# Kernel tuning notes

Measured on AMD Instinct MI355X. Metric: run time of the kernel, lower is better.

Reference implementation:

```python
import jax, jax.numpy as jnp
import numpy as np

EPS = 1e-5
ALPHA = 0.2  # leaky relu negative slope


def instance_norm(x):
    # x: [b, n, c]; torch InstanceNorm1d normalizes each (b, c) over the n dim (no affine)
    mean = jnp.mean(x, axis=1, keepdims=True)
    var = jnp.var(x, axis=1, keepdims=True)
    return (x - mean) * jax.lax.rsqrt(var + EPS)


def gat_layer(x, w, a_src, a_dst, bias):
    # x: [b, n, f_in], w: [h, f_in, f_out], a_src/a_dst: [h, f_out, 1], bias: [f_out]
    h_prime = jnp.einsum('bnf,hfo->bhno', x, w)              # [b, h, n, f_out]
    attn_src = jnp.einsum('bhno,hoi->bhni', h_prime, a_src)[..., 0]  # [b, h, n]
    attn_dst = jnp.einsum('bhno,hoi->bhni', h_prime, a_dst)[..., 0]  # [b, h, n]
    # outer-sum additive attention: attn[b,h,i,j] = src[b,h,i] + dst[b,h,j]
    attn = attn_src[:, :, :, None] + attn_dst[:, :, None, :]
    attn = jnp.where(attn >= 0, attn, ALPHA * attn)          # leaky relu
    attn = jax.nn.softmax(attn, axis=-1)
    out = jnp.einsum('bhnm,bhmo->bhno', attn, h_prime) + bias
    return out


def setup_inputs() -> dict:
    key = jax.random.key(0)
    ks = jax.random.split(key, 9)
    b, n = 16, 1024
    f0, f1, f2 = 32, 16, 32   # n_units
    h0, h1 = 4, 1             # n_heads

    def xavier(k, shape, gain=1.414):
        fan_in, fan_out = shape[-2], shape[-1]
        a = gain * np.sqrt(6.0 / (fan_in + fan_out))
        return jax.random.uniform(k, shape, jnp.float32, -a, a)

    return {
        'x': jax.random.normal(ks[0], (b, n, f0), jnp.float32),
        'w1': xavier(ks[1], (h0, f0, f1)),
        'a_src1': xavier(ks[2], (h0, f1, 1)),
        'a_dst1': xavier(ks[3], (h0, f1, 1)),
        'b1': jnp.zeros((f1,), jnp.float32),
        'w2': xavier(ks[4], (h1, f1 * h0, f2)),
        'a_src2': xavier(ks[5], (h1, f2, 1)),
        'a_dst2': xavier(ks[6], (h1, f2, 1)),
        'b2': jnp.zeros((f2,), jnp.float32),
    }


def reference(x, w1, a_src1, a_dst1, b1, w2, a_src2, a_dst2, b2):
    b, n = x.shape[:2]
    # layer 0
    x = instance_norm(x)
    out = gat_layer(x, w1, a_src1, a_dst1, b1)               # [b, h0, n, f1]
    x = jnp.transpose(out, (0, 2, 1, 3)).reshape(b, n, -1)   # [b, n, h0*f1]
    x = jax.nn.elu(x)
    # layer 1 (last): squeeze head dim
    x = instance_norm(x)
    out = gat_layer(x, w2, a_src2, a_dst2, b2)               # [b, 1, n, f2]
    return out[:, 0]                                          # [b, n, f2]
```

## Files before the change

### kernel.cpp

```cpp
#include <hip/hip_runtime.h>


namespace {
constexpr int Nn  = 1024;
constexpr int F0  = 32;
constexpr int F1n = 16;
constexpr int FH  = 64;
constexpr int F2n = 32;
constexpr float LOG2E = 1.4426950408889634f;
constexpr float EPS   = 1e-5f;
constexpr float ALPHA = 0.2f;
}

typedef __attribute__((ext_vector_type(8))) _Float16 half8;
typedef __attribute__((ext_vector_type(4))) float f32x4;

union alignas(16) Smem {
  struct { float sum[8][33], ssq[8][33], mean[32], rstd[32], wt[2048], as[64], ad[64]; } p1;
  struct { float dst[Nn], red[4], ps[4][16]; } p2;
  struct { float mean[64], rstd[64], wt[2048], as[32], ad[32], sd[4][64][2]; } p3;
  struct { float dst[Nn], red[4], comb[3][64][9], ps[16]; } p4;
};

__device__ __forceinline__ void grid_barrier(unsigned* c, unsigned nblk) {
  __syncthreads();
  if (threadIdx.x == 0) {
    __threadfence();
    __hip_atomic_fetch_add(c, 1u, __ATOMIC_RELAXED, __HIP_MEMORY_SCOPE_AGENT);
    while (__hip_atomic_load(c, __ATOMIC_RELAXED, __HIP_MEMORY_SCOPE_AGENT) < nblk)
      __builtin_amdgcn_s_sleep(2);
    __threadfence();
  }
  __syncthreads();
}

__device__ __forceinline__ void proj1_body(
    int bid, int t, Smem& sm,
    const float* __restrict__ x, const float* __restrict__ w1,
    const float* __restrict__ asrc, const float* __restrict__ adst,
    short* __restrict__ hpT_hi, short* __restrict__ hpT_lo,
    float* __restrict__ src, float* __restrict__ dst,
    float* __restrict__ statsAcc)
{
  const int b    = bid >> 4;
  const int tile = bid & 15;
  const int r    = t & 63, h = t >> 6;

  if (tile == 0 && t < 128) statsAcc[b * 128 + t] = 0.f;

  for (int idx = t; idx < 4 * F1n * F0; idx += 256) {
    const int f = idx & 31, ho = idx >> 5;
    sm.p1.wt[idx] = w1[((ho >> 4) * F0 + f) * F1n + (ho & 15)];
  }
  if (t < 64) { sm.p1.as[t] = asrc[t]; sm.p1.ad[t] = adst[t]; }

  const float* xb = x + (size_t)b * Nn * F0;
  {
    const int c = t & 31, seg = t >> 5;
    float sum = 0.f, ssq = 0.f;
#pragma unroll 8
    for (int nn = seg; nn < Nn; nn += 8) {
      float v = xb[nn * F0 + c];
      sum += v; ssq += v * v;
    }
    sm.p1.sum[seg][c] = sum; sm.p1.ssq[seg][c] = ssq;
  }
  __syncthreads();
  if (t < 32) {
    float s = 0.f, q = 0.f;
#pragma unroll
    for (int k = 0; k < 8; k++) { s += sm.p1.sum[k][t]; q += sm.p1.ssq[k][t]; }
    const float mean = s * (1.f / Nn);
    const float var  = fmaf(-mean, mean, q * (1.f / Nn));
    sm.p1.mean[t] = mean;
    sm.p1.rstd[t] = rsqrtf(var + EPS);
  }
  __syncthreads();

  const int n  = tile * 64 + r;
  const int bh = b * 4 + h;
  float4 xr[F0 / 4];
  const float4* xrow = reinterpret_cast<const float4*>(xb + (size_t)n * F0);
#pragma unroll
  for (int k = 0; k < F0 / 4; k++) {
    float4 v = xrow[k];
    v.x = (v.x - sm.p1.mean[k * 4 + 0]) * sm.p1.rstd[k * 4 + 0];
    v.y = (v.y - sm.p1.mean[k * 4 + 1]) * sm.p1.rstd[k * 4 + 1];
    v.z = (v.z - sm.p1.mean[k * 4 + 2]) * sm.p1.rstd[k * 4 + 2];
    v.w = (v.w - sm.p1.mean[k * 4 + 3]) * sm.p1.rstd[k * 4 + 3];
    xr[k] = v;
  }

  const float4* wt4 = reinterpret_cast<const float4*>(sm.p1.wt);
  float sdot = 0.f, ddot = 0.f;
#pragma unroll 1
  for (int o = 0; o < F1n; o++) {
    float acc = 0.f;
#pragma unroll
    for (int k = 0; k < F0 / 4; k++) {
      const float4 wv = wt4[(h * F1n + o) * (F0 / 4) + k];
      const float4 xv = xr[k];
      acc = fmaf(xv.x, wv.x, acc); acc = fmaf(xv.y, wv.y, acc);
      acc = fmaf(xv.z, wv.z, acc); acc = fmaf(xv.w, wv.w, acc);
    }
    sdot = fmaf(acc, sm.p1.as[h * F1n + o], sdot);
    ddot = fmaf(acc, sm.p1.ad[h * F1n + o], ddot);
    const _Float16 hh = (_Float16)acc;
    const _Float16 hl = (_Float16)(acc - (float)hh);
    const size_t idx = ((size_t)bh * F1n + o) * Nn + n;
    hpT_hi[idx] = __builtin_bit_cast(short, hh);
    hpT_lo[idx] = __builtin_bit_cast(short, hl);
  }
  src[bh * Nn + n] = sdot;
  dst[bh * Nn + n] = ddot;
}

__device__ __forceinline__ void attn1_body(
    int bid, int t, Smem& sm,
    const short* __restrict__ hpT_hi, const short* __restrict__ hpT_lo,
    const float* __restrict__ src, const float* __restrict__ dst,
    const float* __restrict__ bias, float* __restrict__ x1,
    float* __restrict__ statsAcc)
{
  const int bh   = bid >> 4;
  const int tile = bid & 15;
  const int w    = t >> 6;
  const int l    = t & 63;
  const int col  = l & 15;
  const int ks   = l >> 4;

  const float* dp = dst + bh * Nn;
  float lm = -1e30f;
  for (int j = t; j < Nn; j += 256) { float v = dp[j]; sm.p2.dst[j] = v; lm = fmaxf(lm, v); }
#pragma unroll
  for (int mask = 32; mask >= 1; mask >>= 1) lm = fmaxf(lm, __shfl_xor(lm, mask));
  if (l == 0) sm.p2.red[w] = lm;
  __syncthreads();
  const float dmax = fmaxf(fmaxf(sm.p2.red[0], sm.p2.red[1]),
                           fmaxf(sm.p2.red[2], sm.p2.red[3]));

  const int i0 = tile * 64 + w * 16;
  const float si = src[bh * Nn + i0 + col];
  const float t0v = si + dmax;
  const float em  = fmaxf(t0v, ALPHA * t0v) * LOG2E;

  auto pexp = [&](float dv) {
    const float tt = si + dv;
    const float u  = fmaxf(tt, ALPHA * tt);
    return exp2f(fmaf(u, LOG2E, -em));
  };

  const half8* bph = reinterpret_cast<const half8*>(hpT_hi + (size_t)bh * F1n * Nn);
  const half8* bpl = reinterpret_cast<const half8*>(hpT_lo + (size_t)bh * F1n * Nn);
  f32x4 acc = {0.f, 0.f, 0.f, 0.f};
  float psum = 0.f;

#pragma unroll 2
  for (int jb = 0; jb < 32; ++jb) {
    const int jo = (jb << 5) | (ks << 3);
    const float4 dA = *reinterpret_cast<const float4*>(&sm.p2.dst[jo]);
    const float4 dB = *reinterpret_cast<const float4*>(&sm.p2.dst[jo + 4]);
    half8 af;
    const _Float16 q0 = (_Float16)pexp(dA.x); af[0] = q0;
    const _Float16 q1 = (_Float16)pexp(dA.y); af[1] = q1;
    const _Float16 q2 = (_Float16)pexp(dA.z); af[2] = q2;
    const _Float16 q3 = (_Float16)pexp(dA.w); af[3] = q3;
    const _Float16 q4 = (_Float16)pexp(dB.x); af[4] = q4;
    const _Float16 q5 = (_Float16)pexp(dB.y); af[5] = q5;
    const _Float16 q6 = (_Float16)pexp(dB.z); af[6] = q6;
    const _Float16 q7 = (_Float16)pexp(dB.w); af[7] = q7;
    psum += (((float)q0 + (float)q1) + ((float)q2 + (float)q3)) +
            (((float)q4 + (float)q5) + ((float)q6 + (float)q7));

    const half8 bh8 = bph[col * 128 + (jb << 2) + ks];
    const half8 bl8 = bpl[col * 128 + (jb << 2) + ks];
    acc = __builtin_amdgcn_mfma_f32_16x16x32_f16(af, bh8, acc, 0, 0, 0);
    acc = __builtin_amdgcn_mfma_f32_16x16x32_f16(af, bl8, acc, 0, 0, 0);
  }

  psum += __shfl_xor(psum, 16);
  psum += __shfl_xor(psum, 32);
  if (l < 16) sm.p2.ps[w][col] = psum;
  __syncthreads();

  const int b = bh >> 2, h = bh & 3;
  const float bc = bias[col];
  float sv = 0.f, sq = 0.f;
#pragma unroll
  for (int r = 0; r < 4; ++r) {
    const int row = ks * 4 + r;
    const float inv = 1.f / sm.p2.ps[w][row];
    float v = fmaf(acc[r], inv, bc);
    v = v > 0.f ? v : exp2f(v * LOG2E) - 1.f;
    x1[((size_t)(b * Nn + i0 + row)) * FH + h * F1n + col] = v;
    sv += v; sq += v * v;
  }
  sv += __shfl_xor(sv, 16); sq += __shfl_xor(sq, 16);
  sv += __shfl_xor(sv, 32); sq += __shfl_xor(sq, 32);
  if (l < 16) {
    const int ch = h * F1n + col;
    atomicAdd(&statsAcc[b * 128 + ch], sv);
    atomicAdd(&statsAcc[b * 128 + 64 + ch], sq);
  }
}

__device__ __forceinline__ void proj2_body(
    int bid, int t, Smem& sm,
    const float* __restrict__ x1, const float* __restrict__ statsAcc,
    const float* __restrict__ w2,
    const float* __restrict__ asrc, const float* __restrict__ adst,
    short* __restrict__ hpT_hi, short* __restrict__ hpT_lo,
    float* __restrict__ src, float* __restrict__ dst)
{
  const int b    = bid >> 4;
  const int tile = bid & 15;
  const int r    = t & 63, og = t >> 6;

  for (int idx = t; idx < F2n * FH; idx += 256) {
    const int f = idx & 63, o = idx >> 6;
    sm.p3.wt[idx] = w2[f * F2n + o];
  }
  if (t < F2n) { sm.p3.as[t] = asrc[t]; sm.p3.ad[t] = adst[t]; }
  if (t < 64) {
    const float s = statsAcc[b * 128 + t];
    const float q = statsAcc[b * 128 + 64 + t];
    const float mean = s * (1.f / Nn);
    const float var  = fmaf(-mean, mean, q * (1.f / Nn));
    sm.p3.mean[t] = mean;
    sm.p3.rstd[t] = rsqrtf(var + EPS);
  }
  __syncthreads();

  const int n    = tile * 64 + r;
  const int base = b * Nn + n;
  float4 xr[FH / 4];
  const float4* xrow = reinterpret_cast<const float4*>(
      x1 + (size_t)b * Nn * FH + (size_t)n * FH);
#pragma unroll
  for (int k = 0; k < FH / 4; k++) {
    float4 v = xrow[k];
    v.x = (v.x - sm.p3.mean[k * 4 + 0]) * sm.p3.rstd[k * 4 + 0];
    v.y = (v.y - sm.p3.mean[k * 4 + 1]) * sm.p3.rstd[k * 4 + 1];
    v.z = (v.z - sm.p3.mean[k * 4 + 2]) * sm.p3.rstd[k * 4 + 2];
    v.w = (v.w - sm.p3.mean[k * 4 + 3]) * sm.p3.rstd[k * 4 + 3];
    xr[k] = v;
  }

  const float4* wt4 = reinterpret_cast<const float4*>(sm.p3.wt);
  float sdot = 0.f, ddot = 0.f;
#pragma unroll 1
  for (int oo = 0; oo < 8; oo++) {
    const int o = og * 8 + oo;
    float acc = 0.f;
#pragma unroll
    for (int k = 0; k < FH / 4; k++) {
      const float4 wv = wt4[o * (FH / 4) + k];
      const float4 xv = xr[k];
      acc = fmaf(xv.x, wv.x, acc); acc = fmaf(xv.y, wv.y, acc);
      acc = fmaf(xv.z, wv.z, acc); acc = fmaf(xv.w, wv.w, acc);
    }
    sdot = fmaf(acc, sm.p3.as[o], sdot);
    ddot = fmaf(acc, sm.p3.ad[o], ddot);
    const _Float16 hh = (_Float16)acc;
    const _Float16 hl = (_Float16)(acc - (float)hh);
    const size_t idx = ((size_t)b * F2n + o) * Nn + n;
    hpT_hi[idx] = __builtin_bit_cast(short, hh);
    hpT_lo[idx] = __builtin_bit_cast(short, hl);
  }

  sm.p3.sd[og][r][0] = sdot; sm.p3.sd[og][r][1] = ddot;
  __syncthreads();
  if (og == 0) {
    float s = 0.f, d = 0.f;
#pragma unroll
    for (int g = 0; g < 4; g++) { s += sm.p3.sd[g][r][0]; d += sm.p3.sd[g][r][1]; }
    src[base] = s;
    dst[base] = d;
  }
}

__device__ __forceinline__ void attn2_body(
    int bid, int t, Smem& sm,
    const short* __restrict__ hpT_hi, const short* __restrict__ hpT_lo,
    const float* __restrict__ src, const float* __restrict__ dst,
    const float* __restrict__ bias, float* __restrict__ out)
{
  const int b    = bid >> 6;
  const int tile = bid & 63;
  const int jq   = t >> 6;
  const int l    = t & 63;
  const int col  = l & 15;
  const int ks   = l >> 4;

  const float* dp = dst + b * Nn;
  float lm = -1e30f;
  for (int j = t; j < Nn; j += 256) { float v = dp[j]; sm.p4.dst[j] = v; lm = fmaxf(lm, v); }
#pragma unroll
  for (int mask = 32; mask >= 1; mask >>= 1) lm = fmaxf(lm, __shfl_xor(lm, mask));
  if (l == 0) sm.p4.red[jq] = lm;
  __syncthreads();
  const float dmax = fmaxf(fmaxf(sm.p4.red[0], sm.p4.red[1]),
                           fmaxf(sm.p4.red[2], sm.p4.red[3]));

  const int i0 = tile * 16;
  const float si = src[b * Nn + i0 + col];
  const float t0v = si + dmax;
  const float em  = fmaxf(t0v, ALPHA * t0v) * LOG2E;

  auto pexp = [&](float dv) {
    const float tt = si + dv;
    const float u  = fmaxf(tt, ALPHA * tt);
    return exp2f(fmaf(u, LOG2E, -em));
  };

  const half8* bph = reinterpret_cast<const half8*>(hpT_hi + (size_t)b * F2n * Nn);
  const half8* bpl = reinterpret_cast<const half8*>(hpT_lo + (size_t)b * F2n * Nn);
  f32x4 acc0 = {0.f, 0.f, 0.f, 0.f};
  f32x4 acc1 = {0.f, 0.f, 0.f, 0.f};
  float psum = 0.f;

#pragma unroll 2
  for (int kb = 0; kb < 8; ++kb) {
    const int jb = jq * 8 + kb;
    const int jo = (jb << 5) | (ks << 3);
    const float4 dA = *reinterpret_cast<const float4*>(&sm.p4.dst[jo]);
    const float4 dB = *reinterpret_cast<const float4*>(&sm.p4.dst[jo + 4]);
    half8 af;
    const _Float16 q0 = (_Float16)pexp(dA.x); af[0] = q0;
    const _Float16 q1 = (_Float16)pexp(dA.y); af[1] = q1;
    const _Float16 q2 = (_Float16)pexp(dA.z); af[2] = q2;
    const _Float16 q3 = (_Float16)pexp(dA.w); af[3] = q3;
    const _Float16 q4 = (_Float16)pexp(dB.x); af[4] = q4;
    const _Float16 q5 = (_Float16)pexp(dB.y); af[5] = q5;
    const _Float16 q6 = (_Float16)pexp(dB.z); af[6] = q6;
    const _Float16 q7 = (_Float16)pexp(dB.w); af[7] = q7;
    psum += (((float)q0 + (float)q1) + ((float)q2 + (float)q3)) +
            (((float)q4 + (float)q5) + ((float)q6 + (float)q7));

    const half8 bh0 = bph[col * 128 + (jb << 2) + ks];
    const half8 bl0 = bpl[col * 128 + (jb << 2) + ks];
    const half8 bh1 = bph[(col + 16) * 128 + (jb << 2) + ks];
    const half8 bl1 = bpl[(col + 16) * 128 + (jb << 2) + ks];
    acc0 = __builtin_amdgcn_mfma_f32_16x16x32_f16(af, bh0, acc0, 0, 0, 0);
    acc0 = __builtin_amdgcn_mfma_f32_16x16x32_f16(af, bl0, acc0, 0, 0, 0);
    acc1 = __builtin_amdgcn_mfma_f32_16x16x32_f16(af, bh1, acc1, 0, 0, 0);
    acc1 = __builtin_amdgcn_mfma_f32_16x16x32_f16(af, bl1, acc1, 0, 0, 0);
  }

  if (jq > 0) {
#pragma unroll
    for (int r = 0; r < 4; ++r) {
      sm.p4.comb[jq - 1][l][r]     = acc0[r];
      sm.p4.comb[jq - 1][l][r + 4] = acc1[r];
    }
    sm.p4.comb[jq - 1][l][8] = psum;
  }
  __syncthreads();

  if (jq == 0) {
#pragma unroll
    for (int g = 0; g < 3; ++g) {
#pragma unroll
      for (int r = 0; r < 4; ++r) {
        acc0[r] += sm.p4.comb[g][l][r];
        acc1[r] += sm.p4.comb[g][l][r + 4];
      }
      psum += sm.p4.comb[g][l][8];
    }
    psum += __shfl_xor(psum, 16);
    psum += __shfl_xor(psum, 32);
    if (l < 16) sm.p4.ps[col] = psum;

    const float bc0 = bias[col];
    const float bc1 = bias[col + 16];
#pragma unroll
    for (int r = 0; r < 4; ++r) {
      const int row = ks * 4 + r;
      const float inv = 1.f / sm.p4.ps[row];
      float* op = out + ((size_t)(b * Nn + i0 + row)) * F2n;
      op[col]      = fmaf(acc0[r], inv, bc0);
      op[col + 16] = fmaf(acc1[r], inv, bc1);
    }
  }
}

__global__ __launch_bounds__(256, 4) void k_fused(
    const float* __restrict__ x, const float* __restrict__ w1,
    const float* __restrict__ as1, const float* __restrict__ ad1,
    const float* __restrict__ b1,  const float* __restrict__ w2,
    const float* __restrict__ as2, const float* __restrict__ ad2,
    const float* __restrict__ b2,
    short* hpT1_hi, short* hpT1_lo, short* hpT2_hi, short* hpT2_lo,
    float* x1, float* src1, float* dst1, float* src2, float* dst2,
    float* statsA, float* out, unsigned* bars)
{
  __shared__ Smem sm;
  const int bid = blockIdx.x, t = threadIdx.x;

  if (bid < 256)
    proj1_body(bid, t, sm, x, w1, as1, ad1, hpT1_hi, hpT1_lo, src1, dst1, statsA);
  grid_barrier(bars + 0, 1024u);

  attn1_body(bid, t, sm, hpT1_hi, hpT1_lo, src1, dst1, b1, x1, statsA);
  grid_barrier(bars + 1, 1024u);

  if (bid < 256)
    proj2_body(bid, t, sm, x1, statsA, w2, as2, ad2, hpT2_hi, hpT2_lo, src2, dst2);
  grid_barrier(bars + 2, 1024u);

  attn2_body(bid, t, sm, hpT2_hi, hpT2_lo, src2, dst2, b2, out);
}

__global__ __launch_bounds__(256) void k_proj1(
    const float* x, const float* w1, const float* as1, const float* ad1,
    short* hpT_hi, short* hpT_lo, float* src, float* dst, float* statsA)
{ __shared__ Smem sm; proj1_body(blockIdx.x, threadIdx.x, sm, x, w1, as1, ad1, hpT_hi, hpT_lo, src, dst, statsA); }

__global__ __launch_bounds__(256) void k_attn1(
    const short* hpT_hi, const short* hpT_lo, const float* src, const float* dst,
    const float* bias, float* x1, float* statsA)
{ __shared__ Smem sm; attn1_body(blockIdx.x, threadIdx.x, sm, hpT_hi, hpT_lo, src, dst, bias, x1, statsA); }

__global__ __launch_bounds__(256) void k_proj2(
    const float* x1, const float* statsA, const float* w2,
    const float* as2, const float* ad2,
    short* hpT_hi, short* hpT_lo, float* src, float* dst)
{ __shared__ Smem sm; proj2_body(blockIdx.x, threadIdx.x, sm, x1, statsA, w2, as2, ad2, hpT_hi, hpT_lo, src, dst); }

__global__ __launch_bounds__(256) void k_attn2(
    const short* hpT_hi, const short* hpT_lo, const float* src, const float* dst,
    const float* bias, float* out)
{ __shared__ Smem sm; attn2_body(blockIdx.x, threadIdx.x, sm, hpT_hi, hpT_lo, src, dst, bias, out); }

extern "C" void kernel_launch(void* const* d_in, const int* in_sizes, int n_in,
                              void* d_out, int out_size, void* d_ws, size_t ws_size,
                              hipStream_t stream) {
  (void)in_sizes; (void)n_in; (void)out_size; (void)ws_size;
  const float* x   = (const float*)d_in[0];
  const float* w1  = (const float*)d_in[1];
  const float* as1 = (const float*)d_in[2];
  const float* ad1 = (const float*)d_in[3];
  const float* b1  = (const float*)d_in[4];
  const float* w2  = (const float*)d_in[5];
  const float* as2 = (const float*)d_in[6];
  const float* ad2 = (const float*)d_in[7];
  const float* b2  = (const float*)d_in[8];
  float* out = (float*)d_out;

  float* ws = (float*)d_ws;
  short* hpT1_hi = (short*)ws;
  short* hpT1_lo = (short*)(ws + 524288);
  short* hpT2_hi = (short*)(ws + 1048576);
  short* hpT2_lo = (short*)(ws + 1048576 + 262144);
  float* x1      = ws + 1048576 + 524288;
  float* src1    = x1 + 1048576;
  float* dst1    = src1 + 65536;
  float* src2    = dst1 + 65536;
  float* dst2    = src2 + 16384;
  float* statsA  = dst2 + 16384;
  unsigned* bars = (unsigned*)(statsA + 2048);

  (void)hipMemsetAsync(bars, 0, 3 * sizeof(unsigned), stream);

  int maxB = 0;
  hipError_t e = hipOccupancyMaxActiveBlocksPerMultiprocessor(&maxB, k_fused, 256, 0);
  if (e == hipSuccess && maxB >= 4) {
    k_fused<<<1024, 256, 0, stream>>>(x, w1, as1, ad1, b1, w2, as2, ad2, b2,
                                      hpT1_hi, hpT1_lo, hpT2_hi, hpT2_lo,
                                      x1, src1, dst1, src2, dst2, statsA, out, bars);
  } else {
    k_proj1<<<256, 256, 0, stream>>>(x, w1, as1, ad1, hpT1_hi, hpT1_lo, src1, dst1, statsA);
    k_attn1<<<1024, 256, 0, stream>>>(hpT1_hi, hpT1_lo, src1, dst1, b1, x1, statsA);
    k_proj2<<<256, 256, 0, stream>>>(x1, statsA, w2, as2, ad2, hpT2_hi, hpT2_lo, src2, dst2);
    k_attn2<<<1024, 256, 0, stream>>>(hpT2_hi, hpT2_lo, src2, dst2, b2, out);
  }
}
```

Baseline: 146.0 us.

## Replace grid-wide barriers with per-batch barriers and spread projections over all blocks

The fused kernel's three grid-wide barriers over 1024 blocks become per-batch barriers, each counting only the 64 blocks of one batch, with counters padded 32 words apart. Blocks of a batch can then move to the next phase without waiting for the whole grid. Both projection phases now run on all 1024 blocks at 16 rows each, instead of 256 blocks at 64 rows, so no blocks sit idle. Each block stages its normalized rows in shared memory and reduces partial attention dots with wave shuffles. In exchange, every block still recomputes the instance-norm statistics over the full batch, which means four times as many redundant reads of the inputs.

```diff
diff --git a/kernel.cpp b/kernel.cpp
--- a/kernel.cpp
+++ b/kernel.cpp
@@ -16,37 +16,35 @@
 typedef __attribute__((ext_vector_type(4))) float f32x4;
 
 union alignas(16) Smem {
-  struct { float sum[8][33], ssq[8][33], mean[32], rstd[32], wt[2048], as[64], ad[64]; } p1;
+  struct { float sum[8][33], ssq[8][33], mean[32], rstd[32], wt[2048], as[64], ad[64], x[16][33]; } p1;
   struct { float dst[Nn], red[4], ps[4][16]; } p2;
-  struct { float mean[64], rstd[64], wt[2048], as[32], ad[32], sd[4][64][2]; } p3;
+  struct { float mean[64], rstd[64], wt[2048], as[32], ad[32], x[16][65]; } p3;
   struct { float dst[Nn], red[4], comb[3][64][9], ps[16]; } p4;
 };
 
-__device__ __forceinline__ void grid_barrier(unsigned* c, unsigned nblk) {
+__device__ __forceinline__ void batch_barrier(unsigned* c) {
   __syncthreads();
   if (threadIdx.x == 0) {
     __threadfence();
     __hip_atomic_fetch_add(c, 1u, __ATOMIC_RELAXED, __HIP_MEMORY_SCOPE_AGENT);
-    while (__hip_atomic_load(c, __ATOMIC_RELAXED, __HIP_MEMORY_SCOPE_AGENT) < nblk)
-      __builtin_amdgcn_s_sleep(2);
+    while (__hip_atomic_load(c, __ATOMIC_RELAXED, __HIP_MEMORY_SCOPE_AGENT) < 64u)
+      __builtin_amdgcn_s_sleep(1);
     __threadfence();
   }
   __syncthreads();
 }
 
 __device__ __forceinline__ void proj1_body(
-    int bid, int t, Smem& sm,
+    int b, int u, int t, Smem& sm,
     const float* __restrict__ x, const float* __restrict__ w1,
     const float* __restrict__ asrc, const float* __restrict__ adst,
     short* __restrict__ hpT_hi, short* __restrict__ hpT_lo,
     float* __restrict__ src, float* __restrict__ dst,
     float* __restrict__ statsAcc)
 {
-  const int b    = bid >> 4;
-  const int tile = bid & 15;
-  const int r    = t & 63, h = t >> 6;
-
-  if (tile == 0 && t < 128) statsAcc[b * 128 + t] = 0.f;
+  const int r = t >> 4, h = (t >> 2) & 3, dup = t & 3;
+
+  if (u == 0 && t < 128) statsAcc[b * 128 + t] = 0.f;
 
   for (int idx = t; idx < 4 * F1n * F0; idx += 256) {
     const int f = idx & 31, ho = idx >> 5;
@@ -77,61 +75,56 @@
   }
   __syncthreads();
 
-  const int n  = tile * 64 + r;
+  const int n0 = u * 16;
+  for (int idx = t; idx < 16 * F0; idx += 256) {
+    const int rr = idx >> 5, f = idx & 31;
+    sm.p1.x[rr][f] = (xb[(n0 + rr) * F0 + f] - sm.p1.mean[f]) * sm.p1.rstd[f];
+  }
+  __syncthreads();
+
+  const int n  = n0 + r;
   const int bh = b * 4 + h;
-  float4 xr[F0 / 4];
-  const float4* xrow = reinterpret_cast<const float4*>(xb + (size_t)n * F0);
-#pragma unroll
-  for (int k = 0; k < F0 / 4; k++) {
-    float4 v = xrow[k];
-    v.x = (v.x - sm.p1.mean[k * 4 + 0]) * sm.p1.rstd[k * 4 + 0];
-    v.y = (v.y - sm.p1.mean[k * 4 + 1]) * sm.p1.rstd[k * 4 + 1];
-    v.z = (v.z - sm.p1.mean[k * 4 + 2]) * sm.p1.rstd[k * 4 + 2];
-    v.w = (v.w - sm.p1.mean[k * 4 + 3]) * sm.p1.rstd[k * 4 + 3];
-    xr[k] = v;
-  }
-
-  const float4* wt4 = reinterpret_cast<const float4*>(sm.p1.wt);
-  float sdot = 0.f, ddot = 0.f;
-#pragma unroll 1
-  for (int o = 0; o < F1n; o++) {
+  float sp = 0.f, dp = 0.f;
+#pragma unroll
+  for (int k = 0; k < 4; k++) {
+    const int o = dup * 4 + k;
     float acc = 0.f;
 #pragma unroll
-    for (int k = 0; k < F0 / 4; k++) {
-      const float4 wv = wt4[(h * F1n + o) * (F0 / 4) + k];
-      const float4 xv = xr[k];
-      acc = fmaf(xv.x, wv.x, acc); acc = fmaf(xv.y, wv.y, acc);
-      acc = fmaf(xv.z, wv.z, acc); acc = fmaf(xv.w, wv.w, acc);
-    }
-    sdot = fmaf(acc, sm.p1.as[h * F1n + o], sdot);
-    ddot = fmaf(acc, sm.p1.ad[h * F1n + o], ddot);
+    for (int f = 0; f < F0; f++)
+      acc = fmaf(sm.p1.x[r][f], sm.p1.wt[(h * F1n + o) * F0 + f], acc);
+    sp = fmaf(acc, sm.p1.as[h * F1n + o], sp);
+    dp = fmaf(acc, sm.p1.ad[h * F1n + o], dp);
     const _Float16 hh = (_Float16)acc;
     const _Float16 hl = (_Float16)(acc - (float)hh);
     const size_t idx = ((size_t)bh * F1n + o) * Nn + n;
     hpT_hi[idx] = __builtin_bit_cast(short, hh);
     hpT_lo[idx] = __builtin_bit_cast(short, hl);
   }
-  src[bh * Nn + n] = sdot;
-  dst[bh * Nn + n] = ddot;
+  sp += __shfl_xor(sp, 1); dp += __shfl_xor(dp, 1);
+  sp += __shfl_xor(sp, 2); dp += __shfl_xor(dp, 2);
+  if (dup == 0) {
+    src[bh * Nn + n] = sp;
+    dst[bh * Nn + n] = dp;
+  }
 }
 
 __device__ __forceinline__ void attn1_body(
-    int bid, int t, Smem& sm,
+    int b, int u, int t, Smem& sm,
     const short* __restrict__ hpT_hi, const short* __restrict__ hpT_lo,
     const float* __restrict__ src, const float* __restrict__ dst,
     const float* __restrict__ bias, float* __restrict__ x1,
     float* __restrict__ statsAcc)
 {
-  const int bh   = bid >> 4;
-  const int tile = bid & 15;
+  const int bh   = b * 4 + (u >> 4);
+  const int tile = u & 15;
   const int w    = t >> 6;
   const int l    = t & 63;
   const int col  = l & 15;
   const int ks   = l >> 4;
 
-  const float* dp = dst + bh * Nn;
+  const float* dptr = dst + bh * Nn;
   float lm = -1e30f;
-  for (int j = t; j < Nn; j += 256) { float v = dp[j]; sm.p2.dst[j] = v; lm = fmaxf(lm, v); }
+  for (int j = t; j < Nn; j += 256) { float v = dptr[j]; sm.p2.dst[j] = v; lm = fmaxf(lm, v); }
 #pragma unroll
   for (int mask = 32; mask >= 1; mask >>= 1) lm = fmaxf(lm, __shfl_xor(lm, mask));
   if (l == 0) sm.p2.red[w] = lm;
@@ -146,8 +139,8 @@
 
   auto pexp = [&](float dv) {
     const float tt = si + dv;
-    const float u  = fmaxf(tt, ALPHA * tt);
-    return exp2f(fmaf(u, LOG2E, -em));
+    const float uu = fmaxf(tt, ALPHA * tt);
+    return exp2f(fmaf(uu, LOG2E, -em));
   };
 
   const half8* bph = reinterpret_cast<const half8*>(hpT_hi + (size_t)bh * F1n * Nn);
@@ -183,7 +176,7 @@
   if (l < 16) sm.p2.ps[w][col] = psum;
   __syncthreads();
 
-  const int b = bh >> 2, h = bh & 3;
+  const int h = u >> 4;
   const float bc = bias[col];
   float sv = 0.f, sq = 0.f;
 #pragma unroll
@@ -205,16 +198,14 @@
 }
 
 __device__ __forceinline__ void proj2_body(
-    int bid, int t, Smem& sm,
+    int b, int u, int t, Smem& sm,
     const float* __restrict__ x1, const float* __restrict__ statsAcc,
     const float* __restrict__ w2,
     const float* __restrict__ asrc, const float* __restrict__ adst,
     short* __restrict__ hpT_hi, short* __restrict__ hpT_lo,
     float* __restrict__ src, float* __restrict__ dst)
 {
-  const int b    = bid >> 4;
-  const int tile = bid & 15;
-  const int r    = t & 63, og = t >> 6;
+  const int r = t >> 4, g = t & 15;
 
   for (int idx = t; idx < F2n * FH; idx += 256) {
     const int f = idx & 63, o = idx >> 6;
@@ -231,70 +222,56 @@
   }
   __syncthreads();
 
-  const int n    = tile * 64 + r;
+  const int n0 = u * 16;
+  for (int idx = t; idx < 16 * FH; idx += 256) {
+    const int rr = idx >> 6, f = idx & 63;
+    sm.p3.x[rr][f] = (x1[((size_t)(b * Nn + n0 + rr)) * FH + f] - sm.p3.mean[f]) * sm.p3.rstd[f];
+  }
+  __syncthreads();
+
+  const int n    = n0 + r;
   const int base = b * Nn + n;
-  float4 xr[FH / 4];
-  const float4* xrow = reinterpret_cast<const float4*>(
-      x1 + (size_t)b * Nn * FH + (size_t)n * FH);
-#pragma unroll
-  for (int k = 0; k < FH / 4; k++) {
-    float4 v = xrow[k];
-    v.x = (v.x - sm.p3.mean[k * 4 + 0]) * sm.p3.rstd[k * 4 + 0];
-    v.y = (v.y - sm.p3.mean[k * 4 + 1]) * sm.p3.rstd[k * 4 + 1];
-    v.z = (v.z - sm.p3.mean[k * 4 + 2]) * sm.p3.rstd[k * 4 + 2];
-    v.w = (v.w - sm.p3.mean[k * 4 + 3]) * sm.p3.rstd[k * 4 + 3];
-    xr[k] = v;
-  }
-
-  const float4* wt4 = reinterpret_cast<const float4*>(sm.p3.wt);
-  float sdot = 0.f, ddot = 0.f;
-#pragma unroll 1
-  for (int oo = 0; oo < 8; oo++) {
-    const int o = og * 8 + oo;
+  float sp = 0.f, dp = 0.f;
+#pragma unroll
+  for (int k = 0; k < 2; k++) {
+    const int o = g * 2 + k;
     float acc = 0.f;
 #pragma unroll
-    for (int k = 0; k < FH / 4; k++) {
-      const float4 wv = wt4[o * (FH / 4) + k];
-      const float4 xv = xr[k];
-      acc = fmaf(xv.x, wv.x, acc); acc = fmaf(xv.y, wv.y, acc);
-      acc = fmaf(xv.z, wv.z, acc); acc = fmaf(xv.w, wv.w, acc);
-    }
-    sdot = fmaf(acc, sm.p3.as[o], sdot);
-    ddot = fmaf(acc, sm.p3.ad[o], ddot);
+    for (int f = 0; f < FH; f++)
+      acc = fmaf(sm.p3.x[r][f], sm.p3.wt[o * FH + f], acc);
+    sp = fmaf(acc, sm.p3.as[o], sp);
+    dp = fmaf(acc, sm.p3.ad[o], dp);
     const _Float16 hh = (_Float16)acc;
     const _Float16 hl = (_Float16)(acc - (float)hh);
     const size_t idx = ((size_t)b * F2n + o) * Nn + n;
     hpT_hi[idx] = __builtin_bit_cast(short, hh);
     hpT_lo[idx] = __builtin_bit_cast(short, hl);
   }
-
-  sm.p3.sd[og][r][0] = sdot; sm.p3.sd[og][r][1] = ddot;
-  __syncthreads();
-  if (og == 0) {
-    float s = 0.f, d = 0.f;
-#pragma unroll
-    for (int g = 0; g < 4; g++) { s += sm.p3.sd[g][r][0]; d += sm.p3.sd[g][r][1]; }
-    src[base] = s;
-    dst[base] = d;
+  sp += __shfl_xor(sp, 1); dp += __shfl_xor(dp, 1);
+  sp += __shfl_xor(sp, 2); dp += __shfl_xor(dp, 2);
+  sp += __shfl_xor(sp, 4); dp += __shfl_xor(dp, 4);
+  sp += __shfl_xor(sp, 8); dp += __shfl_xor(dp, 8);
+  if (g == 0) {
+    src[base] = sp;
+    dst[base] = dp;
   }
 }
 
 __device__ __forceinline__ void attn2_body(
-    int bid, int t, Smem& sm,
+    int b, int u, int t, Smem& sm,
     const short* __restrict__ hpT_hi, const short* __restrict__ hpT_lo,
     const float* __restrict__ src, const float* __restrict__ dst,
     const float* __restrict__ bias, float* __restrict__ out)
 {
-  const int b    = bid >> 6;
-  const int tile = bid & 63;
+  const int tile = u;
   const int jq   = t >> 6;
   const int l    = t & 63;
   const int col  = l & 15;
   const int ks   = l >> 4;
 
-  const float* dp = dst + b * Nn;
+  const float* dptr = dst + b * Nn;
   float lm = -1e30f;
-  for (int j = t; j < Nn; j += 256) { float v = dp[j]; sm.p4.dst[j] = v; lm = fmaxf(lm, v); }
+  for (int j = t; j < Nn; j += 256) { float v = dptr[j]; sm.p4.dst[j] = v; lm = fmaxf(lm, v); }
 #pragma unroll
   for (int mask = 32; mask >= 1; mask >>= 1) lm = fmaxf(lm, __shfl_xor(lm, mask));
   if (l == 0) sm.p4.red[jq] = lm;
@@ -309,8 +286,8 @@
 
   auto pexp = [&](float dv) {
     const float tt = si + dv;
-    const float u  = fmaxf(tt, ALPHA * tt);
-    return exp2f(fmaf(u, LOG2E, -em));
+    const float uu = fmaxf(tt, ALPHA * tt);
+    return exp2f(fmaf(uu, LOG2E, -em));
   };
 
   const half8* bph = reinterpret_cast<const half8*>(hpT_hi + (size_t)b * F2n * Nn);
@@ -396,41 +373,40 @@
 {
   __shared__ Smem sm;
   const int bid = blockIdx.x, t = threadIdx.x;
-
-  if (bid < 256)
-    proj1_body(bid, t, sm, x, w1, as1, ad1, hpT1_hi, hpT1_lo, src1, dst1, statsA);
-  grid_barrier(bars + 0, 1024u);
-
-  attn1_body(bid, t, sm, hpT1_hi, hpT1_lo, src1, dst1, b1, x1, statsA);
-  grid_barrier(bars + 1, 1024u);
-
-  if (bid < 256)
-    proj2_body(bid, t, sm, x1, statsA, w2, as2, ad2, hpT2_hi, hpT2_lo, src2, dst2);
-  grid_barrier(bars + 2, 1024u);
-
-  attn2_body(bid, t, sm, hpT2_hi, hpT2_lo, src2, dst2, b2, out);
+  const int b = bid >> 6, u = bid & 63;
+
+  proj1_body(b, u, t, sm, x, w1, as1, ad1, hpT1_hi, hpT1_lo, src1, dst1, statsA);
+  batch_barrier(bars + ((0 * 16 + b) << 5));
+
+  attn1_body(b, u, t, sm, hpT1_hi, hpT1_lo, src1, dst1, b1, x1, statsA);
+  batch_barrier(bars + ((1 * 16 + b) << 5));
+
+  proj2_body(b, u, t, sm, x1, statsA, w2, as2, ad2, hpT2_hi, hpT2_lo, src2, dst2);
+  batch_barrier(bars + ((2 * 16 + b) << 5));
+
+  attn2_body(b, u, t, sm, hpT2_hi, hpT2_lo, src2, dst2, b2, out);
 }
 
 __global__ __launch_bounds__(256) void k_proj1(
     const float* x, const float* w1, const float* as1, const float* ad1,
     short* hpT_hi, short* hpT_lo, float* src, float* dst, float* statsA)
-{ __shared__ Smem sm; proj1_body(blockIdx.x, threadIdx.x, sm, x, w1, as1, ad1, hpT_hi, hpT_lo, src, dst, statsA); }
+{ __shared__ Smem sm; proj1_body(blockIdx.x >> 6, blockIdx.x & 63, threadIdx.x, sm, x, w1, as1, ad1, hpT_hi, hpT_lo, src, dst, statsA); }
 
 __global__ __launch_bounds__(256) void k_attn1(
     const short* hpT_hi, const short* hpT_lo, const float* src, const float* dst,
     const float* bias, float* x1, float* statsA)
-{ __shared__ Smem sm; attn1_body(blockIdx.x, threadIdx.x, sm, hpT_hi, hpT_lo, src, dst, bias, x1, statsA); }
+{ __shared__ Smem sm; attn1_body(blockIdx.x >> 6, blockIdx.x & 63, threadIdx.x, sm, hpT_hi, hpT_lo, src, dst, bias, x1, statsA); }
 
 __global__ __launch_bounds__(256) void k_proj2(
     const float* x1, const float* statsA, const float* w2,
     const float* as2, const float* ad2,
     short* hpT_hi, short* hpT_lo, float* src, float* dst)
-{ __shared__ Smem sm; proj2_body(blockIdx.x, threadIdx.x, sm, x1, statsA, w2, as2, ad2, hpT_hi, hpT_lo, src, dst); }
+{ __shared__ Smem sm; proj2_body(blockIdx.x >> 6, blockIdx.x & 63, threadIdx.x, sm, x1, statsA, w2, as2, ad2, hpT_hi, hpT_lo, src, dst); }
 
 __global__ __launch_bounds__(256) void k_attn2(
     const short* hpT_hi, const short* hpT_lo, const float* src, const float* dst,
     const float* bias, float* out)
-{ __shared__ Smem sm; attn2_body(blockIdx.x, threadIdx.x, sm, hpT_hi, hpT_lo, src, dst, bias, out); }
+{ __shared__ Smem sm; attn2_body(blockIdx.x >> 6, blockIdx.x & 63, threadIdx.x, sm, hpT_hi, hpT_lo, src, dst, bias, out); }
 
 extern "C" void kernel_launch(void* const* d_in, const int* in_sizes, int n_in,
                               void* d_out, int out_size, void* d_ws, size_t ws_size,
@@ -460,7 +436,7 @@
   float* statsA  = dst2 + 16384;
   unsigned* bars = (unsigned*)(statsA + 2048);
 
-  (void)hipMemsetAsync(bars, 0, 3 * sizeof(unsigned), stream);
+  (void)hipMemsetAsync(bars, 0, 3 * 16 * 32 * sizeof(unsigned), stream);
 
   int maxB = 0;
   hipError_t e = hipOccupancyMaxActiveBlocksPerMultiprocessor(&maxB, k_fused, 256, 0);
@@ -469,9 +445,9 @@
                                       hpT1_hi, hpT1_lo, hpT2_hi, hpT2_lo,
                                       x1, src1, dst1, src2, dst2, statsA, out, bars);
   } else {
-    k_proj1<<<256, 256, 0, stream>>>(x, w1, as1, ad1, hpT1_hi, hpT1_lo, src1, dst1, statsA);
+    k_proj1<<<1024, 256, 0, stream>>>(x, w1, as1, ad1, hpT1_hi, hpT1_lo, src1, dst1, statsA);
     k_attn1<<<1024, 256, 0, stream>>>(hpT1_hi, hpT1_lo, src1, dst1, b1, x1, statsA);
-    k_proj2<<<256, 256, 0, stream>>>(x1, statsA, w2, as2, ad2, hpT2_hi, hpT2_lo, src2, dst2);
+    k_proj2<<<1024, 256, 0, stream>>>(x1, statsA, w2, as2, ad2, hpT2_hi, hpT2_lo, src2, dst2);
     k_attn2<<<1024, 256, 0, stream>>>(hpT2_hi, hpT2_lo, src2, dst2, b2, out);
   }
 }
```

Measured after the change: 171.9 us. 1.18x slower.
